# Kernel optimization log

Measured on AMD Instinct MI355X. Metric: run time of the kernel, lower is better.

Reference implementation:

```python
import jax, jax.numpy as jnp
import numpy as np

E, L, D, H, S, B = 8, 12, 768, 12, 512, 32
DIMS = [12, 8, 8, 8, 8, 12]
RANKS = [1, 8, 8, 8, 8, 8, 1]
ALPHA = 8.0


def setup_inputs() -> dict:
    key = jax.random.key(0)
    ks = iter(jax.random.split(key, 32))
    inp = {}
    inp['hidden_states'] = jax.random.normal(next(ks), (B, S, D), jnp.float32)
    inp['router_weights'] = jax.random.normal(next(ks), (D, E), jnp.float32)
    for pre in ('q', 'v'):
        for i in range(6):
            shp = (E, L, RANKS[i], DIMS[i], RANKS[i + 1])
            inp[f'{pre}_core{i}'] = jax.random.normal(next(ks), shp, jnp.float32) * 0.05
    for nm in ('Wq', 'Wk', 'Wv', 'Wo'):
        inp[nm] = jax.random.normal(next(ks), (L, D, D), jnp.float32) * 0.02
    for nm in ('bq', 'bk', 'bv', 'bo'):
        inp[nm] = jnp.zeros((L, D), jnp.float32)
    inp['ln_scale'] = jnp.ones((L, D), jnp.float32)
    inp['ln_bias'] = jnp.zeros((L, D), jnp.float32)
    return inp


def _layernorm(x, scale, bias, eps=1e-12):
    mu = x.mean(-1, keepdims=True)
    var = ((x - mu) ** 2).mean(-1, keepdims=True)
    return (x - mu) * jax.lax.rsqrt(var + eps) * scale + bias


def _tt_weights(cores):
    # cores[i]: [L, r_i, d_i, r_{i+1}]; chained TT contraction, vectorized over layers
    w = jnp.einsum('Lijk,Lklm,Lmno,Lopq,Lqrs,Lstu->Ljlnprt', *cores)
    return w.reshape(w.shape[0], D, D)  # [L, out, in] (matches torch weight.reshape)


def reference(hidden_states, router_weights,
              q_core0, q_core1, q_core2, q_core3, q_core4, q_core5,
              v_core0, v_core1, v_core2, v_core3, v_core4, v_core5,
              Wq, Wk, Wv, Wo, bq, bk, bv, bo, ln_scale, ln_bias):
    # routing: pool over sequence, softmax + argmax per sample
    pooled = hidden_states.mean(axis=1)                      # [B, D]
    probs = jax.nn.softmax(pooled @ router_weights, axis=-1)  # [B, E]
    idx = jnp.argmax(probs, axis=-1)                          # [B]
    e = idx[-1]
    qc = [c[e] for c in (q_core0, q_core1, q_core2, q_core3, q_core4, q_core5)]
    vc = [c[e] for c in (v_core0, v_core1, v_core2, v_core3, v_core4, v_core5)]
    Wq_a = Wq + ALPHA * _tt_weights(qc)  # [L, D, D]
    Wv_a = Wv + ALPHA * _tt_weights(vc)

    hd = D // H
    scale = 1.0 / jnp.sqrt(jnp.float32(hd))
    x = hidden_states
    for l in range(L):
        q = (x @ Wq_a[l].T + bq[l]).reshape(B, S, H, hd)
        k = (x @ Wk[l].T + bk[l]).reshape(B, S, H, hd)
        v = (x @ Wv_a[l].T + bv[l]).reshape(B, S, H, hd)
        scores = jnp.einsum('bqhd,bkhd->bhqk', q, k) * scale
        attn = jax.nn.softmax(scores, axis=-1)
        ctx = jnp.einsum('bhqk,bkhd->bqhd', attn, v).reshape(B, S, D)
        out = ctx @ Wo[l].T + bo[l]
        x = _layernorm(x + out, ln_scale[l], ln_bias[l])
    return x
```

## Files before the change

kernel.cpp:

```cpp
#include <hip/hip_runtime.h>
#include <hip/hip_bf16.h>
#include <stdint.h>

#define E_ 8
#define L_ 12
#define D_ 768
#define H_ 12
#define S_ 512
#define B_ 32
#define BS_ (B_*S_)

typedef __attribute__((ext_vector_type(4))) float floatx4;
typedef __attribute__((ext_vector_type(8))) __bf16 bf16x8;
typedef __attribute__((ext_vector_type(4))) __bf16 bf16x4;

__device__ __forceinline__ __bf16 f2bf(float f) {
  unsigned u = __builtin_bit_cast(unsigned, f);
  u += 0x7fffu + ((u >> 16) & 1u);
  unsigned short h = (unsigned short)(u >> 16);
  return __builtin_bit_cast(__bf16, h);
}

__device__ __forceinline__ float fexp2(float x) {
#if __has_builtin(__builtin_amdgcn_exp2f)
  return __builtin_amdgcn_exp2f(x);
#else
  return exp2f(x);
#endif
}

__device__ __forceinline__ void async16(const void* g, void* l) {
  __builtin_amdgcn_global_load_lds((__attribute__((address_space(1))) void*)g,
                                   (__attribute__((address_space(3))) void*)l,
                                   16, 0, 0);
}

__global__ void routing_pool_kernel(const float* __restrict__ hidden,
                                    float* __restrict__ partial) {
  const int blk = blockIdx.x;
  const int tid = threadIdx.x;
  const float* base = hidden + (size_t)(B_-1)*S_*D_ + (size_t)blk*8*D_;
  float acc[3] = {0.f, 0.f, 0.f};
  for (int s = 0; s < 8; ++s) {
#pragma unroll
    for (int i = 0; i < 3; ++i)
      acc[i] += base[(size_t)s*D_ + tid + i*256];
  }
#pragma unroll
  for (int i = 0; i < 3; ++i) partial[(size_t)blk*D_ + tid + i*256] = acc[i];
}

__global__ void routing_finish_kernel(const float* __restrict__ partial,
                                      const float* __restrict__ rw,
                                      int* __restrict__ e_out) {
  __shared__ float pooled[D_];
  __shared__ float logits[E_];
  int tid = threadIdx.x;
#pragma unroll
  for (int i = 0; i < 3; ++i) {
    int d = tid + i*256;
    float s = 0.f;
    for (int blk = 0; blk < 64; ++blk) s += partial[(size_t)blk*D_ + d];
    pooled[d] = s;
  }
  __syncthreads();
  if (tid < E_) {
    float s = 0.f;
    for (int d = 0; d < D_; ++d) s += pooled[d] * rw[d*E_ + tid];
    logits[tid] = s;
  }
  __syncthreads();
  if (tid == 0) {
    int best = 0; float bvv = logits[0];
    for (int e = 1; e < E_; ++e) if (logits[e] > bvv) { bvv = logits[e]; best = e; }
    e_out[0] = best;
  }
}

__global__ void convert_bf16_kernel(const float* __restrict__ src, __bf16* __restrict__ dst) {
  size_t i = ((size_t)blockIdx.x*256 + threadIdx.x)*8;
  __bf16 r[8];
#pragma unroll
  for (int j = 0; j < 8; ++j) r[j] = f2bf(src[i+j]);
  *(bf16x8*)(dst + i) = *(bf16x8*)r;
}

__global__ void convert_wk_kernel(const float* __restrict__ wk, __bf16* __restrict__ wqkv) {
  size_t i = ((size_t)blockIdx.x*256 + threadIdx.x)*8;
  int l = (int)(i / (D_*D_));
  int rem = (int)(i % (D_*D_));
  int n = rem / D_, k = rem % D_;
  __bf16 r[8];
#pragma unroll
  for (int j = 0; j < 8; ++j) r[j] = f2bf(wk[i+j]);
  *(bf16x8*)(wqkv + (size_t)l*2304*D_ + (size_t)(768+n)*D_ + k) = *(bf16x8*)r;
}

__global__ void tt_prep_kernel(
    const float* __restrict__ qc0, const float* __restrict__ qc1, const float* __restrict__ qc2,
    const float* __restrict__ qc3, const float* __restrict__ qc4, const float* __restrict__ qc5,
    const float* __restrict__ vc0, const float* __restrict__ vc1, const float* __restrict__ vc2,
    const float* __restrict__ vc3, const float* __restrict__ vc4, const float* __restrict__ vc5,
    const float* __restrict__ Wq, const float* __restrict__ Wv,
    const int* __restrict__ e_idx, __bf16* __restrict__ wqkv) {
  const int l = blockIdx.x;
  const int pre = blockIdx.y;
  const int z = blockIdx.z;
  const int tid = threadIdx.x;
  const int e = e_idx[0];
  const float* c0 = (pre ? vc0 : qc0) + (size_t)(e*L_ + l)*96;
  const float* c1 = (pre ? vc1 : qc1) + (size_t)(e*L_ + l)*512;
  const float* c2 = (pre ? vc2 : qc2) + (size_t)(e*L_ + l)*512;
  const float* c3 = (pre ? vc3 : qc3) + (size_t)(e*L_ + l)*512;
  const float* c4 = (pre ? vc4 : qc4) + (size_t)(e*L_ + l)*512;
  const float* c5 = (pre ? vc5 : qc5) + (size_t)(e*L_ + l)*96;
  __shared__ float M1[768];
  __shared__ float R2[768];
  __shared__ float M2[6144];
  __shared__ float Rm[6144];
  for (int idx = tid; idx < 768; idx += 256) {
    int j = idx >> 6, rem = idx & 63, l2 = rem >> 3, m = rem & 7;
    float s = 0.f;
    for (int k = 0; k < 8; ++k) s += c0[j*8 + k] * c1[k*64 + l2*8 + m];
    M1[idx] = s;
    int qq = idx / 96, rem2 = idx % 96, rr = rem2 / 12, t = rem2 % 12;
    float s2 = 0.f;
    for (int si = 0; si < 8; ++si) s2 += c4[qq*64 + rr*8 + si] * c5[si*12 + t];
    R2[idx] = s2;
  }
  __syncthreads();
  for (int idx = tid; idx < 6144; idx += 256) {
    int o = idx & 7, n = (idx >> 3) & 7, jl = idx >> 6;
    float s = 0.f;
    for (int m = 0; m < 8; ++m) s += M1[jl*8 + m] * c2[m*64 + n*8 + o];
    M2[idx] = s;
    int o2 = idx / 768, inp = idx % 768, p = inp / 96, rt = inp % 96;
    float s2 = 0.f;
    for (int qq = 0; qq < 8; ++qq) s2 += c3[o2*64 + p*8 + qq] * R2[qq*96 + rt];
    Rm[idx] = s2;
  }
  __syncthreads();
  const float* Wbase = (pre ? Wv : Wq) + (size_t)l*D_*D_;
  __bf16* dst = wqkv + (size_t)l*2304*D_ + (pre ? (size_t)1536*D_ : 0);
  for (int g = tid; g < 48*96; g += 256) {
    const int outr = z*48 + (g / 96);
    const int inp0 = (g % 96) * 8;
    float m2r[8];
#pragma unroll
    for (int o = 0; o < 8; ++o) m2r[o] = M2[outr*8 + o];
    float acc[8];
#pragma unroll
    for (int u = 0; u < 8; ++u) acc[u] = 0.f;
#pragma unroll
    for (int o = 0; o < 8; ++o) {
      float4 r0 = *(const float4*)&Rm[o*768 + inp0];
      float4 r1 = *(const float4*)&Rm[o*768 + inp0 + 4];
      acc[0] += m2r[o]*r0.x; acc[1] += m2r[o]*r0.y;
      acc[2] += m2r[o]*r0.z; acc[3] += m2r[o]*r0.w;
      acc[4] += m2r[o]*r1.x; acc[5] += m2r[o]*r1.y;
      acc[6] += m2r[o]*r1.z; acc[7] += m2r[o]*r1.w;
    }
    const float* wb = Wbase + (size_t)outr*768 + inp0;
    float4 w0 = *(const float4*)wb;
    float4 w1 = *(const float4*)(wb + 4);
    __bf16 r[8];
    r[0] = f2bf(w0.x + 8.f*acc[0]); r[1] = f2bf(w0.y + 8.f*acc[1]);
    r[2] = f2bf(w0.z + 8.f*acc[2]); r[3] = f2bf(w0.w + 8.f*acc[3]);
    r[4] = f2bf(w1.x + 8.f*acc[4]); r[5] = f2bf(w1.y + 8.f*acc[5]);
    r[6] = f2bf(w1.z + 8.f*acc[6]); r[7] = f2bf(w1.w + 8.f*acc[7]);
    *(bf16x8*)(dst + (size_t)outr*768 + inp0) = *(bf16x8*)r;
  }
}

#define SLOT_BYTES 28672
template<bool SPLITV>
__global__ __launch_bounds__(512, 2) void gemm_bt(
    const __bf16* __restrict__ A, const __bf16* __restrict__ Bw,
    const float* __restrict__ bq, const float* __restrict__ bk, const float* __restrict__ bvp,
    __bf16* __restrict__ outb, __bf16* __restrict__ vtout, int Nw) {
  __shared__ __align__(16) char lds[4*SLOT_BYTES];
  const int tid = threadIdx.x;
  const int w = tid >> 6, lane = tid & 63;
  const int quad = lane >> 4, l16 = lane & 15;
  const int wm = w >> 2, wn = w & 3;
  const size_t mblk = (size_t)blockIdx.y * 256;
  const size_t nblk = (size_t)blockIdx.x * 192;
  const __bf16* Ag = A + mblk * 768;
  const __bf16* Bg = Bw + nblk * 768;

  int a_goff[2], a_loff[2];
#pragma unroll
  for (int i = 0; i < 2; ++i) {
    int line = w*16 + i*8 + (lane >> 3);
    int s8 = (lane & 7) ^ (line & 7);
    int row = 2*line + (s8 >> 2);
    a_goff[i] = row*768 + (s8 & 3)*8;
    a_loff[i] = (w*16 + i*8)*128;
  }
  int b_goff[2], b_loff[2];
#pragma unroll
  for (int i = 0; i < 2; ++i) {
    int bl0 = (w < 4) ? (w*16 + i*8) : (64 + (w-4)*8);
    int line = bl0 + (lane >> 3);
    int s8 = (lane & 7) ^ (line & 7);
    int row = 2*line + (s8 >> 2);
    b_goff[i] = row*768 + (s8 & 3)*8;
    b_loff[i] = 16384 + bl0*128;
  }

  int a_foff[8], b_foff[3];
#pragma unroll
  for (int mf = 0; mf < 8; ++mf) {
    int r = wm*128 + mf*16 + l16;
    int line = r >> 1, s8 = (r & 1)*4 + quad, ph = s8 ^ (line & 7);
    a_foff[mf] = line*128 + ph*16;
  }
#pragma unroll
  for (int nf = 0; nf < 3; ++nf) {
    int r = wn*48 + nf*16 + l16;
    int line = r >> 1, s8 = (r & 1)*4 + quad, ph = s8 ^ (line & 7);
    b_foff[nf] = 16384 + line*128 + ph*16;
  }

  floatx4 acc[8][3];
#pragma unroll
  for (int mf = 0; mf < 8; ++mf)
#pragma unroll
    for (int nf = 0; nf < 3; ++nf) acc[mf][nf] = {0.f,0.f,0.f,0.f};

  auto STAGE = [&](int t) {
    const __bf16* Ab = Ag + t*32;
    const __bf16* Bb = Bg + t*32;
    char* ls = lds + (t & 3)*SLOT_BYTES;
    async16(Ab + a_goff[0], ls + a_loff[0]);
    async16(Ab + a_goff[1], ls + a_loff[1]);
    if (w < 4) {
      async16(Bb + b_goff[0], ls + b_loff[0]);
      async16(Bb + b_goff[1], ls + b_loff[1]);
    } else {
      async16(Bb + b_goff[0], ls + b_loff[0]);
    }
  };

  auto COMPUTE = [&](int t) {
    const char* ls = lds + (t & 3)*SLOT_BYTES;
    bf16x8 af[8], bfr[3];
#pragma unroll
    for (int mf = 0; mf < 8; ++mf) af[mf] = *(const bf16x8*)(ls + a_foff[mf]);
#pragma unroll
    for (int nf = 0; nf < 3; ++nf) bfr[nf] = *(const bf16x8*)(ls + b_foff[nf]);
    __builtin_amdgcn_s_setprio(1);
#pragma unroll
    for (int mf = 0; mf < 8; ++mf)
#pragma unroll
      for (int nf = 0; nf < 3; ++nf)
        acc[mf][nf] = __builtin_amdgcn_mfma_f32_16x16x32_bf16(af[mf], bfr[nf], acc[mf][nf], 0, 0, 0);
    __builtin_amdgcn_s_setprio(0);
  };

  STAGE(0); STAGE(1); STAGE(2);
  for (int t = 0; t < 22; ++t) {
    if (w < 4) asm volatile("s_waitcnt vmcnt(8)" ::: "memory");
    else       asm volatile("s_waitcnt vmcnt(6)" ::: "memory");
    __builtin_amdgcn_s_barrier();
    if (t < 21) STAGE(t + 3);
    COMPUTE(t);
  }
  if (w < 4) asm volatile("s_waitcnt vmcnt(4)" ::: "memory");
  else       asm volatile("s_waitcnt vmcnt(3)" ::: "memory");
  __builtin_amdgcn_s_barrier();
  COMPUTE(22);
  asm volatile("s_waitcnt vmcnt(0)" ::: "memory");
  __builtin_amdgcn_s_barrier();
  COMPUTE(23);

  if (SPLITV && blockIdx.x >= 8) {
#pragma unroll
    for (int nf = 0; nf < 3; ++nf) {
      const int vcol = (int)nblk - 1536 + wn*48 + nf*16 + l16;
      const int h = vcol >> 6, d = vcol & 63;
      const float bval = bvp[vcol];
#pragma unroll
      for (int mf = 0; mf < 8; ++mf) {
        const int mrow = (int)mblk + wm*128 + mf*16 + quad*4;
        const int b = mrow >> 9, s = mrow & 511;
        __bf16 pr[4];
#pragma unroll
        for (int r = 0; r < 4; ++r) pr[r] = f2bf(acc[mf][nf][r] + bval);
        *(bf16x4*)(vtout + (size_t)((b*H_ + h)*64 + d)*S_ + s) = *(bf16x4*)pr;
      }
    }
    return;
  }
  const float* bias = bq;
  if (SPLITV) bias = (blockIdx.x < 4) ? bq : bk;
  float bval[3]; int ncol[3];
#pragma unroll
  for (int nf = 0; nf < 3; ++nf) {
    ncol[nf] = (int)nblk + wn*48 + nf*16 + l16;
    int bc = ncol[nf]; if (bc >= 768) bc -= 768;
    bval[nf] = bias[bc];
  }
#pragma unroll
  for (int mf = 0; mf < 8; ++mf) {
#pragma unroll
    for (int nf = 0; nf < 3; ++nf) {
#pragma unroll
      for (int r = 0; r < 4; ++r) {
        const int mrow = (int)mblk + wm*128 + mf*16 + quad*4 + r;
        outb[(size_t)mrow*Nw + ncol[nf]] = f2bf(acc[mf][nf][r] + bval[nf]);
      }
    }
  }
}

#define PSTR 72
__global__ __launch_bounds__(256) void flash_kernel(const __bf16* __restrict__ qkv,
                                                    const __bf16* __restrict__ vt,
                                                    __bf16* __restrict__ ctx) {
  __shared__ __align__(16) __bf16 Qs[64*PSTR];
  __shared__ __align__(16) __bf16 Ks[64*PSTR];
  __shared__ __align__(16) __bf16 Vts[64*PSTR];
  __shared__ __align__(16) __bf16 Ps[64*PSTR];
  const int tid = threadIdx.x;
  const int w = tid >> 6, lane = tid & 63;
  const int quad = lane >> 4, l16 = lane & 15;
  const int n = blockIdx.x;
  const int bh = (n >> 6)*8 + (n & 7);
  const int q0 = ((n >> 3) & 7) * 64;
  const int b = bh / H_, h = bh % H_;
  const float SCL = 0.125f * 1.44269504f;

  {
#pragma unroll
    for (int it = 0; it < 2; ++it) {
      int slot = it*256 + tid, row = slot >> 3, seg = slot & 7;
      bf16x8 v = *(const bf16x8*)(qkv + (size_t)(b*S_ + q0 + row)*2304 + h*64 + seg*8);
      *(bf16x8*)&Qs[row*PSTR + seg*8] = v;
    }
  }

  floatx4 acc_o[4];
#pragma unroll
  for (int jd = 0; jd < 4; ++jd) acc_o[jd] = {0.f,0.f,0.f,0.f};
  float m_prev = -__builtin_inff();
  float l_part = 0.f;

  for (int kt = 0; kt < 8; ++kt) {
    __syncthreads();
#pragma unroll
    for (int it = 0; it < 2; ++it) {
      int slot = it*256 + tid, row = slot >> 3, seg = slot & 7;
      bf16x8 kvv = *(const bf16x8*)(qkv + (size_t)(b*S_ + kt*64 + row)*2304 + 768 + h*64 + seg*8);
      bf16x8 vtv = *(const bf16x8*)(vt + (size_t)(bh*64 + row)*S_ + kt*64 + seg*8);
      *(bf16x8*)&Ks[row*PSTR + seg*8] = kvv;
      *(bf16x8*)&Vts[row*PSTR + seg*8] = vtv;
    }
    __syncthreads();
    floatx4 sacc[4];
#pragma unroll
    for (int i = 0; i < 4; ++i) sacc[i] = {0.f,0.f,0.f,0.f};
#pragma unroll
    for (int kk = 0; kk < 64; kk += 32) {
      bf16x8 bq_ = *(const bf16x8*)&Qs[(w*16 + l16)*PSTR + kk + quad*8];
#pragma unroll
      for (int i = 0; i < 4; ++i) {
        bf16x8 ak = *(const bf16x8*)&Ks[(i*16 + l16)*PSTR + kk + quad*8];
        sacc[i] = __builtin_amdgcn_mfma_f32_16x16x32_bf16(ak, bq_, sacc[i], 0, 0, 0);
      }
    }
    float sv[4][4];
#pragma unroll
    for (int i = 0; i < 4; ++i)
#pragma unroll
      for (int r = 0; r < 4; ++r) sv[i][r] = sacc[i][r] * SCL;
    float mloc = sv[0][0];
#pragma unroll
    for (int i = 0; i < 4; ++i)
#pragma unroll
      for (int r = 0; r < 4; ++r) mloc = fmaxf(mloc, sv[i][r]);
    mloc = fmaxf(mloc, __shfl_xor(mloc, 16));
    mloc = fmaxf(mloc, __shfl_xor(mloc, 32));
    float mnew = fmaxf(m_prev, mloc);
    float alpha = fexp2(m_prev - mnew);
    m_prev = mnew;
    float rsum = 0.f;
#pragma unroll
    for (int i = 0; i < 4; ++i) {
      __bf16 pr[4];
#pragma unroll
      for (int r = 0; r < 4; ++r) {
        float p = fexp2(sv[i][r] - mnew);
        rsum += p;
        pr[r] = f2bf(p);
      }
      *(bf16x4*)&Ps[(w*16 + l16)*PSTR + i*16 + quad*4] = *(bf16x4*)pr;
    }
    l_part = l_part*alpha + rsum;
    float ab[4];
#pragma unroll
    for (int r = 0; r < 4; ++r) ab[r] = __shfl(alpha, quad*4 + r);
#pragma unroll
    for (int jd = 0; jd < 4; ++jd)
#pragma unroll
      for (int r = 0; r < 4; ++r) acc_o[jd][r] *= ab[r];
#pragma unroll
    for (int kk = 0; kk < 64; kk += 32) {
      bf16x8 ap = *(const bf16x8*)&Ps[(w*16 + l16)*PSTR + kk + quad*8];
#pragma unroll
      for (int jd = 0; jd < 4; ++jd) {
        bf16x8 bv_ = *(const bf16x8*)&Vts[(jd*16 + l16)*PSTR + kk + quad*8];
        acc_o[jd] = __builtin_amdgcn_mfma_f32_16x16x32_bf16(ap, bv_, acc_o[jd], 0, 0, 0);
      }
    }
  }
  float l_tot = l_part;
  l_tot += __shfl_xor(l_tot, 16);
  l_tot += __shfl_xor(l_tot, 32);
  float lb[4];
#pragma unroll
  for (int r = 0; r < 4; ++r) lb[r] = __shfl(l_tot, quad*4 + r);
#pragma unroll
  for (int jd = 0; jd < 4; ++jd) {
    const int d = jd*16 + l16;
#pragma unroll
    for (int r = 0; r < 4; ++r) {
      const int q = q0 + w*16 + quad*4 + r;
      ctx[(size_t)(b*S_ + q)*D_ + h*64 + d] = f2bf(acc_o[jd][r] / lb[r]);
    }
  }
}

template<bool FIRST, bool LAST>
__global__ __launch_bounds__(256) void ln_kernel(const float* __restrict__ residf,
                                                 __bf16* xb,
                                                 const __bf16* __restrict__ proj,
                                                 const float* __restrict__ gamma,
                                                 const float* __restrict__ beta,
                                                 float* __restrict__ xoutf) {
  const int tid = threadIdx.x;
  const int w = tid >> 6, lane = tid & 63;
  const int row = blockIdx.x*4 + w;
  const size_t base = (size_t)row * D_;
  const int c0 = lane*8;
  const bool has2 = lane < 32;
  const int c1 = 512 + lane*8;

  float v0[8], v1[8];
  {
    bf16x8 p0 = *(const bf16x8*)(proj + base + c0);
    if (FIRST) {
      float4 a = *(const float4*)(residf + base + c0);
      float4 bq4 = *(const float4*)(residf + base + c0 + 4);
      v0[0]=a.x+(float)p0[0]; v0[1]=a.y+(float)p0[1]; v0[2]=a.z+(float)p0[2]; v0[3]=a.w+(float)p0[3];
      v0[4]=bq4.x+(float)p0[4]; v0[5]=bq4.y+(float)p0[5]; v0[6]=bq4.z+(float)p0[6]; v0[7]=bq4.w+(float)p0[7];
    } else {
      bf16x8 r0 = *(const bf16x8*)(xb + base + c0);
#pragma unroll
      for (int j = 0; j < 8; ++j) v0[j] = (float)r0[j] + (float)p0[j];
    }
    if (has2) {
      bf16x8 p1 = *(const bf16x8*)(proj + base + c1);
      if (FIRST) {
        float4 a = *(const float4*)(residf + base + c1);
        float4 bq4 = *(const float4*)(residf + base + c1 + 4);
        v1[0]=a.x+(float)p1[0]; v1[1]=a.y+(float)p1[1]; v1[2]=a.z+(float)p1[2]; v1[3]=a.w+(float)p1[3];
        v1[4]=bq4.x+(float)p1[4]; v1[5]=bq4.y+(float)p1[5]; v1[6]=bq4.z+(float)p1[6]; v1[7]=bq4.w+(float)p1[7];
      } else {
        bf16x8 r1 = *(const bf16x8*)(xb + base + c1);
#pragma unroll
        for (int j = 0; j < 8; ++j) v1[j] = (float)r1[j] + (float)p1[j];
      }
    } else {
#pragma unroll
      for (int j = 0; j < 8; ++j) v1[j] = 0.f;
    }
  }
  float s = 0.f;
#pragma unroll
  for (int j = 0; j < 8; ++j) s += v0[j] + v1[j];
#pragma unroll
  for (int off = 32; off; off >>= 1) s += __shfl_xor(s, off);
  const float mu = s * (1.f/768.f);
  float q = 0.f;
#pragma unroll
  for (int j = 0; j < 8; ++j) { float d0 = v0[j]-mu; q += d0*d0; }
  if (has2) {
#pragma unroll
    for (int j = 0; j < 8; ++j) { float d1 = v1[j]-mu; q += d1*d1; }
  }
#pragma unroll
  for (int off = 32; off; off >>= 1) q += __shfl_xor(q, off);
  const float rs = rsqrtf(q * (1.f/768.f) + 1e-12f);

  {
    float4 g0 = *(const float4*)(gamma + c0);
    float4 g1 = *(const float4*)(gamma + c0 + 4);
    float4 b0 = *(const float4*)(beta + c0);
    float4 b1 = *(const float4*)(beta + c0 + 4);
    float o[8];
    o[0]=(v0[0]-mu)*rs*g0.x+b0.x; o[1]=(v0[1]-mu)*rs*g0.y+b0.y;
    o[2]=(v0[2]-mu)*rs*g0.z+b0.z; o[3]=(v0[3]-mu)*rs*g0.w+b0.w;
    o[4]=(v0[4]-mu)*rs*g1.x+b1.x; o[5]=(v0[5]-mu)*rs*g1.y+b1.y;
    o[6]=(v0[6]-mu)*rs*g1.z+b1.z; o[7]=(v0[7]-mu)*rs*g1.w+b1.w;
    if (LAST) {
      *(float4*)(xoutf + base + c0)     = {o[0],o[1],o[2],o[3]};
      *(float4*)(xoutf + base + c0 + 4) = {o[4],o[5],o[6],o[7]};
    } else {
      __bf16 ob[8];
#pragma unroll
      for (int j = 0; j < 8; ++j) ob[j] = f2bf(o[j]);
      *(bf16x8*)(xb + base + c0) = *(bf16x8*)ob;
    }
  }
  if (has2) {
    float4 g0 = *(const float4*)(gamma + c1);
    float4 g1 = *(const float4*)(gamma + c1 + 4);
    float4 b0 = *(const float4*)(beta + c1);
    float4 b1 = *(const float4*)(beta + c1 + 4);
    float o[8];
    o[0]=(v1[0]-mu)*rs*g0.x+b0.x; o[1]=(v1[1]-mu)*rs*g0.y+b0.y;
    o[2]=(v1[2]-mu)*rs*g0.z+b0.z; o[3]=(v1[3]-mu)*rs*g0.w+b0.w;
    o[4]=(v1[4]-mu)*rs*g1.x+b1.x; o[5]=(v1[5]-mu)*rs*g1.y+b1.y;
    o[6]=(v1[6]-mu)*rs*g1.z+b1.z; o[7]=(v1[7]-mu)*rs*g1.w+b1.w;
    if (LAST) {
      *(float4*)(xoutf + base + c1)     = {o[0],o[1],o[2],o[3]};
      *(float4*)(xoutf + base + c1 + 4) = {o[4],o[5],o[6],o[7]};
    } else {
      __bf16 ob[8];
#pragma unroll
      for (int j = 0; j < 8; ++j) ob[j] = f2bf(o[j]);
      *(bf16x8*)(xb + base + c1) = *(bf16x8*)ob;
    }
  }
}

extern "C" void kernel_launch(void* const* d_in, const int* in_sizes, int n_in,
                              void* d_out, int out_size, void* d_ws, size_t ws_size,
                              hipStream_t stream) {
  const float* hidden = (const float*)d_in[0];
  const float* router = (const float*)d_in[1];
  const float* qc[6]; const float* vc[6];
  for (int i = 0; i < 6; ++i) qc[i] = (const float*)d_in[2+i];
  for (int i = 0; i < 6; ++i) vc[i] = (const float*)d_in[8+i];
  const float* Wq = (const float*)d_in[14];
  const float* Wk = (const float*)d_in[15];
  const float* Wv = (const float*)d_in[16];
  const float* Wo = (const float*)d_in[17];
  const float* bq = (const float*)d_in[18];
  const float* bk = (const float*)d_in[19];
  const float* bv = (const float*)d_in[20];
  const float* bo = (const float*)d_in[21];
  const float* lns = (const float*)d_in[22];
  const float* lnb = (const float*)d_in[23];
  float* out = (float*)d_out;

  char* ws = (char*)d_ws;
  size_t off = 0;
  auto alloc = [&](size_t bytes) -> void* {
    off = (off + 255) & ~(size_t)255;
    void* p = ws + off; off += bytes; return p;
  };
  int*    e_idx = (int*)   alloc(4);
  float*  rpart = (float*) alloc((size_t)64*D_*4);
  __bf16* xbf   = (__bf16*)alloc((size_t)BS_*D_*2);
  __bf16* qkv   = (__bf16*)alloc((size_t)BS_*2304*2);
  __bf16* vt    = (__bf16*)alloc((size_t)B_*H_*64*S_*2);
  __bf16* ctx   = (__bf16*)alloc((size_t)BS_*D_*2);
  __bf16* projb = (__bf16*)alloc((size_t)BS_*D_*2);
  __bf16* wqkv  = (__bf16*)alloc((size_t)L_*2304*D_*2);
  __bf16* wobf  = (__bf16*)alloc((size_t)L_*D_*D_*2);
  (void)ws_size; (void)in_sizes; (void)n_in; (void)out_size;

  routing_pool_kernel<<<64, 256, 0, stream>>>(hidden, rpart);
  routing_finish_kernel<<<1, 256, 0, stream>>>(rpart, router, e_idx);
  convert_bf16_kernel<<<(BS_*D_)/2048, 256, 0, stream>>>(hidden, xbf);
  tt_prep_kernel<<<dim3(L_, 2, 16), 256, 0, stream>>>(qc[0],qc[1],qc[2],qc[3],qc[4],qc[5],
                                                      vc[0],vc[1],vc[2],vc[3],vc[4],vc[5],
                                                      Wq, Wv, e_idx, wqkv);
  convert_wk_kernel<<<(L_*D_*D_)/2048, 256, 0, stream>>>(Wk, wqkv);
  convert_bf16_kernel<<<(L_*D_*D_)/2048, 256, 0, stream>>>(Wo, wobf);

  for (int l = 0; l < L_; ++l) {
    gemm_bt<true><<<dim3(12,64), 512, 0, stream>>>(xbf, wqkv + (size_t)l*2304*D_,
        bq + l*D_, bk + l*D_, bv + l*D_, qkv, vt, 2304);
    flash_kernel<<<3072, 256, 0, stream>>>(qkv, vt, ctx);
    gemm_bt<false><<<dim3(4,64), 512, 0, stream>>>(ctx, wobf + (size_t)l*D_*D_,
        bo + l*D_, nullptr, nullptr, projb, nullptr, 768);
    if (l == 0)
      ln_kernel<true,false><<<BS_/4, 256, 0, stream>>>(hidden, xbf, projb,
          lns + l*D_, lnb + l*D_, nullptr);
    else if (l == L_-1)
      ln_kernel<false,true><<<BS_/4, 256, 0, stream>>>(nullptr, xbf, projb,
          lns + l*D_, lnb + l*D_, out);
    else
      ln_kernel<false,false><<<BS_/4, 256, 0, stream>>>(nullptr, xbf, projb,
          lns + l*D_, lnb + l*D_, nullptr);
  }
}
```

Baseline: 2.443 ms.

## Split GEMM main loop into half-step LDS loads interleaved with MFMA

Restructures the projection GEMM inner loop so each K-step issues LDS fragment loads in two halves, with barriers and sched_barrier fences placed so one half's MFMAs overlap the other half's LDS reads and the next async global stage. The goal is to hide LDS read latency behind matrix math and to space out global prefetch issue. It adds an extra barrier per K-step, and the fences constrain the compiler's own scheduling.

```diff
diff --git a/kernel.cpp b/kernel.cpp
--- a/kernel.cpp
+++ b/kernel.cpp
@@ -242,37 +242,70 @@
     }
   };
 
-  auto COMPUTE = [&](int t) {
-    const char* ls = lds + (t & 3)*SLOT_BYTES;
-    bf16x8 af[8], bfr[3];
-#pragma unroll
-    for (int mf = 0; mf < 8; ++mf) af[mf] = *(const bf16x8*)(ls + a_foff[mf]);
+  bf16x8 af[8], bfr[3];
+  auto LOAD1 = [&](int u) {
+    const char* ls = lds + (u & 3)*SLOT_BYTES;
 #pragma unroll
     for (int nf = 0; nf < 3; ++nf) bfr[nf] = *(const bf16x8*)(ls + b_foff[nf]);
+#pragma unroll
+    for (int mf = 0; mf < 4; ++mf) af[mf] = *(const bf16x8*)(ls + a_foff[mf]);
+  };
+  auto LOAD2 = [&](int u) {
+    const char* ls = lds + (u & 3)*SLOT_BYTES;
+#pragma unroll
+    for (int mf = 4; mf < 8; ++mf) af[mf] = *(const bf16x8*)(ls + a_foff[mf]);
+  };
+  auto MM = [&](int mf0) {
     __builtin_amdgcn_s_setprio(1);
 #pragma unroll
-    for (int mf = 0; mf < 8; ++mf)
+    for (int mf = mf0; mf < mf0 + 4; ++mf)
 #pragma unroll
       for (int nf = 0; nf < 3; ++nf)
         acc[mf][nf] = __builtin_amdgcn_mfma_f32_16x16x32_bf16(af[mf], bfr[nf], acc[mf][nf], 0, 0, 0);
     __builtin_amdgcn_s_setprio(0);
   };
+  auto BAR = [&]() {
+    __builtin_amdgcn_s_barrier();
+    __builtin_amdgcn_sched_barrier(0);
+  };
 
   STAGE(0); STAGE(1); STAGE(2);
-  for (int t = 0; t < 22; ++t) {
+  if (w < 4) asm volatile("s_waitcnt vmcnt(8)" ::: "memory");
+  else       asm volatile("s_waitcnt vmcnt(6)" ::: "memory");
+  BAR();
+
+  for (int u = 0; u < 21; ++u) {
+    LOAD1(u);
+    BAR();
+    MM(0);
+    LOAD2(u);
+    STAGE(u + 3);
     if (w < 4) asm volatile("s_waitcnt vmcnt(8)" ::: "memory");
     else       asm volatile("s_waitcnt vmcnt(6)" ::: "memory");
-    __builtin_amdgcn_s_barrier();
-    if (t < 21) STAGE(t + 3);
-    COMPUTE(t);
-  }
+    BAR();
+    MM(4);
+  }
+  LOAD1(21);
+  BAR();
+  MM(0);
+  LOAD2(21);
   if (w < 4) asm volatile("s_waitcnt vmcnt(4)" ::: "memory");
   else       asm volatile("s_waitcnt vmcnt(3)" ::: "memory");
-  __builtin_amdgcn_s_barrier();
-  COMPUTE(22);
+  BAR();
+  MM(4);
+  LOAD1(22);
+  BAR();
+  MM(0);
+  LOAD2(22);
   asm volatile("s_waitcnt vmcnt(0)" ::: "memory");
-  __builtin_amdgcn_s_barrier();
-  COMPUTE(23);
+  BAR();
+  MM(4);
+  LOAD1(23);
+  BAR();
+  MM(0);
+  LOAD2(23);
+  BAR();
+  MM(4);
 
   if (SPLITV && blockIdx.x >= 8) {
 #pragma unroll
```

New measurement: 2.470 ms. Within noise of the previous version (+1.1%).

## Widen GEMM tile to 256x256 with double-buffered LDS staging

Applied to the files above, without the earlier changes.

The bf16 GEMM tile grows from 256x192 to 256x256, so each wave computes 8x4 MFMA fragments instead of 8x3 and the QKV and output-projection grids shrink to 9 and 3 column blocks. Staging moves from a four-slot, three-ahead pipeline to two 32 KB slots: half the waves load A, the other half load B, with a full vmcnt(0) wait and barrier every k-step. The aim is more reuse per LDS byte loaded and fewer blocks. In exchange the prefetch depth drops to one, which may expose global-load latency, and the extra accumulators raise register pressure under the two-blocks-per-CU launch bound.

```diff
diff --git a/kernel.cpp b/kernel.cpp
--- a/kernel.cpp
+++ b/kernel.cpp
@@ -172,43 +172,35 @@
   }
 }
 
-#define SLOT_BYTES 28672
+#define SLOT_BYTES 32768
 template<bool SPLITV>
 __global__ __launch_bounds__(512, 2) void gemm_bt(
     const __bf16* __restrict__ A, const __bf16* __restrict__ Bw,
     const float* __restrict__ bq, const float* __restrict__ bk, const float* __restrict__ bvp,
     __bf16* __restrict__ outb, __bf16* __restrict__ vtout, int Nw) {
-  __shared__ __align__(16) char lds[4*SLOT_BYTES];
+  __shared__ __align__(16) char lds[2*SLOT_BYTES];
   const int tid = threadIdx.x;
   const int w = tid >> 6, lane = tid & 63;
   const int quad = lane >> 4, l16 = lane & 15;
   const int wm = w >> 2, wn = w & 3;
   const size_t mblk = (size_t)blockIdx.y * 256;
-  const size_t nblk = (size_t)blockIdx.x * 192;
+  const size_t nblk = (size_t)blockIdx.x * 256;
   const __bf16* Ag = A + mblk * 768;
   const __bf16* Bg = Bw + nblk * 768;
 
-  int a_goff[2], a_loff[2];
-#pragma unroll
-  for (int i = 0; i < 2; ++i) {
-    int line = w*16 + i*8 + (lane >> 3);
+  const bool stA = (w < 4);
+  int goff[4], loff[4];
+#pragma unroll
+  for (int i = 0; i < 4; ++i) {
+    int lb = (w & 3)*32 + i*8;
+    int line = lb + (lane >> 3);
     int s8 = (lane & 7) ^ (line & 7);
     int row = 2*line + (s8 >> 2);
-    a_goff[i] = row*768 + (s8 & 3)*8;
-    a_loff[i] = (w*16 + i*8)*128;
-  }
-  int b_goff[2], b_loff[2];
-#pragma unroll
-  for (int i = 0; i < 2; ++i) {
-    int bl0 = (w < 4) ? (w*16 + i*8) : (64 + (w-4)*8);
-    int line = bl0 + (lane >> 3);
-    int s8 = (lane & 7) ^ (line & 7);
-    int row = 2*line + (s8 >> 2);
-    b_goff[i] = row*768 + (s8 & 3)*8;
-    b_loff[i] = 16384 + bl0*128;
-  }
-
-  int a_foff[8], b_foff[3];
+    goff[i] = row*768 + (s8 & 3)*8;
+    loff[i] = (stA ? 0 : 16384) + lb*128;
+  }
+
+  int a_foff[8], b_foff[4];
 #pragma unroll
   for (int mf = 0; mf < 8; ++mf) {
     int r = wm*128 + mf*16 + l16;
@@ -216,68 +208,60 @@
     a_foff[mf] = line*128 + ph*16;
   }
 #pragma unroll
-  for (int nf = 0; nf < 3; ++nf) {
-    int r = wn*48 + nf*16 + l16;
+  for (int nf = 0; nf < 4; ++nf) {
+    int r = wn*64 + nf*16 + l16;
     int line = r >> 1, s8 = (r & 1)*4 + quad, ph = s8 ^ (line & 7);
     b_foff[nf] = 16384 + line*128 + ph*16;
   }
 
-  floatx4 acc[8][3];
+  floatx4 acc[8][4];
 #pragma unroll
   for (int mf = 0; mf < 8; ++mf)
 #pragma unroll
-    for (int nf = 0; nf < 3; ++nf) acc[mf][nf] = {0.f,0.f,0.f,0.f};
+    for (int nf = 0; nf < 4; ++nf) acc[mf][nf] = {0.f,0.f,0.f,0.f};
 
   auto STAGE = [&](int t) {
-    const __bf16* Ab = Ag + t*32;
-    const __bf16* Bb = Bg + t*32;
-    char* ls = lds + (t & 3)*SLOT_BYTES;
-    async16(Ab + a_goff[0], ls + a_loff[0]);
-    async16(Ab + a_goff[1], ls + a_loff[1]);
-    if (w < 4) {
-      async16(Bb + b_goff[0], ls + b_loff[0]);
-      async16(Bb + b_goff[1], ls + b_loff[1]);
-    } else {
-      async16(Bb + b_goff[0], ls + b_loff[0]);
-    }
+    const __bf16* Gb = (stA ? Ag : Bg) + t*32;
+    char* ls = lds + (t & 1)*SLOT_BYTES;
+#pragma unroll
+    for (int i = 0; i < 4; ++i) async16(Gb + goff[i], ls + loff[i]);
   };
 
   auto COMPUTE = [&](int t) {
-    const char* ls = lds + (t & 3)*SLOT_BYTES;
-    bf16x8 af[8], bfr[3];
+    const char* ls = lds + (t & 1)*SLOT_BYTES;
+    bf16x8 af[8], bfr[4];
+#pragma unroll
+    for (int nf = 0; nf < 4; ++nf) bfr[nf] = *(const bf16x8*)(ls + b_foff[nf]);
 #pragma unroll
     for (int mf = 0; mf < 8; ++mf) af[mf] = *(const bf16x8*)(ls + a_foff[mf]);
-#pragma unroll
-    for (int nf = 0; nf < 3; ++nf) bfr[nf] = *(const bf16x8*)(ls + b_foff[nf]);
     __builtin_amdgcn_s_setprio(1);
 #pragma unroll
     for (int mf = 0; mf < 8; ++mf)
 #pragma unroll
-      for (int nf = 0; nf < 3; ++nf)
+      for (int nf = 0; nf < 4; ++nf)
         acc[mf][nf] = __builtin_amdgcn_mfma_f32_16x16x32_bf16(af[mf], bfr[nf], acc[mf][nf], 0, 0, 0);
     __builtin_amdgcn_s_setprio(0);
   };
 
-  STAGE(0); STAGE(1); STAGE(2);
-  for (int t = 0; t < 22; ++t) {
-    if (w < 4) asm volatile("s_waitcnt vmcnt(8)" ::: "memory");
-    else       asm volatile("s_waitcnt vmcnt(6)" ::: "memory");
-    __builtin_amdgcn_s_barrier();
-    if (t < 21) STAGE(t + 3);
-    COMPUTE(t);
-  }
-  if (w < 4) asm volatile("s_waitcnt vmcnt(4)" ::: "memory");
-  else       asm volatile("s_waitcnt vmcnt(3)" ::: "memory");
-  __builtin_amdgcn_s_barrier();
-  COMPUTE(22);
+  STAGE(0);
   asm volatile("s_waitcnt vmcnt(0)" ::: "memory");
   __builtin_amdgcn_s_barrier();
-  COMPUTE(23);
-
-  if (SPLITV && blockIdx.x >= 8) {
-#pragma unroll
-    for (int nf = 0; nf < 3; ++nf) {
-      const int vcol = (int)nblk - 1536 + wn*48 + nf*16 + l16;
+  __builtin_amdgcn_sched_barrier(0);
+
+  for (int t = 0; t < 24; ++t) {
+    if (t < 23) STAGE(t + 1);
+    COMPUTE(t);
+    if (t < 23) {
+      asm volatile("s_waitcnt vmcnt(0)" ::: "memory");
+      __builtin_amdgcn_s_barrier();
+      __builtin_amdgcn_sched_barrier(0);
+    }
+  }
+
+  if (SPLITV && blockIdx.x >= 6) {
+#pragma unroll
+    for (int nf = 0; nf < 4; ++nf) {
+      const int vcol = (int)nblk - 1536 + wn*64 + nf*16 + l16;
       const int h = vcol >> 6, d = vcol & 63;
       const float bval = bvp[vcol];
 #pragma unroll
@@ -293,18 +277,18 @@
     return;
   }
   const float* bias = bq;
-  if (SPLITV) bias = (blockIdx.x < 4) ? bq : bk;
-  float bval[3]; int ncol[3];
-#pragma unroll
-  for (int nf = 0; nf < 3; ++nf) {
-    ncol[nf] = (int)nblk + wn*48 + nf*16 + l16;
+  if (SPLITV) bias = (blockIdx.x < 3) ? bq : bk;
+  float bval[4]; int ncol[4];
+#pragma unroll
+  for (int nf = 0; nf < 4; ++nf) {
+    ncol[nf] = (int)nblk + wn*64 + nf*16 + l16;
     int bc = ncol[nf]; if (bc >= 768) bc -= 768;
     bval[nf] = bias[bc];
   }
 #pragma unroll
   for (int mf = 0; mf < 8; ++mf) {
 #pragma unroll
-    for (int nf = 0; nf < 3; ++nf) {
+    for (int nf = 0; nf < 4; ++nf) {
 #pragma unroll
       for (int r = 0; r < 4; ++r) {
         const int mrow = (int)mblk + wm*128 + mf*16 + quad*4 + r;
@@ -582,10 +566,10 @@
   convert_bf16_kernel<<<(L_*D_*D_)/2048, 256, 0, stream>>>(Wo, wobf);
 
   for (int l = 0; l < L_; ++l) {
-    gemm_bt<true><<<dim3(12,64), 512, 0, stream>>>(xbf, wqkv + (size_t)l*2304*D_,
+    gemm_bt<true><<<dim3(9,64), 512, 0, stream>>>(xbf, wqkv + (size_t)l*2304*D_,
         bq + l*D_, bk + l*D_, bv + l*D_, qkv, vt, 2304);
     flash_kernel<<<3072, 256, 0, stream>>>(qkv, vt, ctx);
-    gemm_bt<false><<<dim3(4,64), 512, 0, stream>>>(ctx, wobf + (size_t)l*D_*D_,
+    gemm_bt<false><<<dim3(3,64), 512, 0, stream>>>(ctx, wobf + (size_t)l*D_*D_,
         bo + l*D_, nullptr, nullptr, projb, nullptr, 768);
     if (l == 0)
       ln_kernel<true,false><<<BS_/4, 256, 0, stream>>>(hidden, xbf, projb,
```

New measurement: 2.647 ms. 8.3% more time.
